# Performance work log

Hardware: AMD Instinct MI355X
Metric: run time of the kernel (lower is better)

Reference implementation:

```python
import jax, jax.numpy as jnp
import numpy as np

EPS = 1e-5

def _binact(x):
    # ReActNet piecewise-polynomial sign with straight-through estimator
    p = jnp.where(x < -1.0, -1.0,
        jnp.where(x < 0.0, x * x + 2.0 * x,
        jnp.where(x < 1.0, -x * x + 2.0 * x, 1.0)))
    return jax.lax.stop_gradient(jnp.sign(x) - p) + p

def _binweight(w):
    # per-output-channel scaling * sign(w), STE through clipped weights
    scale = jax.lax.stop_gradient(jnp.mean(jnp.abs(w), axis=(1, 2, 3), keepdims=True))
    bw = scale * jnp.sign(w)
    cl = jnp.clip(w, -1.0, 1.0)
    return jax.lax.stop_gradient(bw - cl) + cl

def _conv(x, w, stride, pad):
    return jax.lax.conv_general_dilated(x, w, (stride, stride), [(pad, pad), (pad, pad)],
                                        dimension_numbers=('NCHW', 'OIHW', 'NCHW'))

def _bn(x, gamma, beta, mean, var):
    inv = gamma / jnp.sqrt(var + EPS)
    return x * inv[None, :, None, None] + (beta - mean * inv)[None, :, None, None]

def _prelu(x, a):
    return jnp.where(x > 0, x, a[None, :, None, None] * x)

def _bias(x, b):
    return x + b[None, :, None, None]

def setup_inputs() -> dict:
    key = jax.random.key(0)
    ks = jax.random.split(key, 12)
    B, C, H, W = 32, 256, 28, 28
    d = {}
    d['x'] = jax.random.normal(ks[0], (B, C, H, W), jnp.float32)
    d['loss'] = jnp.zeros((), jnp.float32)
    # learnable biases (move11/12/13, move21/22/23)
    for i, name in enumerate(['b11', 'b12', 'b13', 'b21', 'b22', 'b23']):
        d[name] = 0.01 * jax.random.normal(ks[1 + i], (C,), jnp.float32)
    # binary conv weights: 3x3 (C->C, groups=1) and 1x1 (C->C)
    d['w1'] = 0.05 * jax.random.normal(ks[7], (C, C, 3, 3), jnp.float32)
    d['w2'] = 0.05 * jax.random.normal(ks[8], (C, C, 1, 1), jnp.float32)
    # batchnorm params (inference-style running stats)
    d['g1'] = jnp.ones((C,), jnp.float32); d['be1'] = jnp.zeros((C,), jnp.float32)
    d['m1'] = 0.1 * jax.random.normal(ks[9], (C,), jnp.float32)
    d['v1'] = 0.5 + jax.random.uniform(ks[10], (C,), jnp.float32)
    d['g2'] = jnp.ones((C,), jnp.float32); d['be2'] = jnp.zeros((C,), jnp.float32)
    d['m2'] = 0.1 * jax.random.normal(ks[11], (C,), jnp.float32)
    d['v2'] = 0.5 + jax.random.uniform(jax.random.fold_in(key, 99), (C,), jnp.float32)
    # PReLU slopes
    d['a1'] = 0.25 * jnp.ones((C,), jnp.float32)
    d['a2'] = 0.25 * jnp.ones((C,), jnp.float32)
    return d

def reference(x, loss, b11, b12, b13, b21, b22, b23, w1, w2,
              g1, be1, m1, v1, g2, be2, m2, v2, a1, a2):
    # branch 1: bias -> sign act -> 3x3 binary conv -> BN -> residual -> bias/PReLU/bias
    out1 = _binact(_bias(x, b11))
    out1 = _conv(out1, _binweight(w1), 1, 1)
    out1 = _bn(out1, g1, be1, m1, v1)
    out1 = out1 + x  # adaptive_add: shapes match (stride=1, inp==oup)
    out1 = _bias(_prelu(_bias(out1, b12), a1), b13)
    # branch 2: bias -> sign act -> 1x1 binary conv -> BN -> residual -> bias/PReLU/bias
    out2 = _binact(_bias(out1, b21))
    out2 = _conv(out2, _binweight(w2), 1, 0)
    out2 = _bn(out2, g2, be2, m2, v2)
    out2 = out2 + out1
    out2 = _bias(_prelu(_bias(out2, b22), a2), b23)
    return (out2, loss)
```

## Files before the change

### kernel.cpp

```cpp
#include <hip/hip_runtime.h>
#include <hip/hip_bf16.h>


typedef unsigned short u16;
typedef unsigned char  u8;
typedef unsigned int   u32;
typedef unsigned long long u64;
typedef float f32x4 __attribute__((ext_vector_type(4)));
typedef long  long2v __attribute__((ext_vector_type(2)));
typedef int   v8i  __attribute__((ext_vector_type(8)));
typedef float v16f __attribute__((ext_vector_type(16)));

__device__ __forceinline__ float b2f(u16 u) {
  union { unsigned int i; float f; } c; c.i = ((unsigned int)u) << 16; return c.f;
}
__device__ __forceinline__ u16 f2b(float f) {
  unsigned int u = __builtin_bit_cast(unsigned int, f);
  unsigned int r = (u + 0x7FFFu + ((u >> 16) & 1u)) >> 16;
  return (u16)r;
}
__device__ __forceinline__ u32 f2sign4(float v) {
  return (v > 0.f) ? 0x2u : ((v < 0.f) ? 0xAu : 0x0u);
}
__device__ __forceinline__ v8i mkv8(long2v a, long2v b) {
  union { long2v l[2]; v8i v; } u; u.l[0] = a; u.l[1] = b; return u.v;
}

__global__ __launch_bounds__(256) void prep_kernel(
    const float* __restrict__ w1, const float* __restrict__ w2,
    const float* __restrict__ g1, const float* __restrict__ be1,
    const float* __restrict__ m1, const float* __restrict__ v1,
    const float* __restrict__ g2, const float* __restrict__ be2,
    const float* __restrict__ m2, const float* __restrict__ v2,
    u8* __restrict__ w1T, u8* __restrict__ w2T,
    float* __restrict__ ab,
    float* __restrict__ lossdst, const float* __restrict__ lossin)
{
  __shared__ float wrow[2304];
  __shared__ float red[256];
  const int t = threadIdx.x;
  const int blk = blockIdx.x;
  float s = 0.f;
  if (blk < 256) {
    const int o = blk;
    const float4* src = (const float4*)(w1 + o * 2304);
#pragma unroll
    for (int i = 0; i < 3; ++i) {
      int c = i * 256 + t;
      if (c < 576) {
        float4 v = src[c];
        wrow[c * 4 + 0] = v.x; wrow[c * 4 + 1] = v.y;
        wrow[c * 4 + 2] = v.z; wrow[c * 4 + 3] = v.w;
        s += fabsf(v.x) + fabsf(v.y) + fabsf(v.z) + fabsf(v.w);
      }
    }
  } else {
    const int o = blk - 256;
    float v = w2[o * 256 + t];
    wrow[t] = v;
    s = fabsf(v);
  }
  red[t] = s;
  __syncthreads();
  for (int st = 128; st > 0; st >>= 1) { if (t < st) red[t] += red[t + st]; __syncthreads(); }
  if (blk < 256) {
    const int o = blk;
    for (int it = t; it < 288; it += 256) {
      int tap = it >> 5, ci8 = it & 31;
      u32 pack = 0;
#pragma unroll
      for (int k = 0; k < 8; ++k)
        pack |= f2sign4(wrow[(ci8 * 8 + k) * 9 + tap]) << (4 * k);
      int c64 = ci8 >> 3, kh = (ci8 >> 2) & 1, slot = ci8 & 3;
      *(u32*)(w1T + (size_t)((tap * 4 + c64) * 2 + kh) * 4096 + o * 16 + slot * 4) = pack;
    }
    if (t == 0) {
      float scale = red[0] / 2304.f;
      float inv = g1[o] / sqrtf(v1[o] + 1e-5f);
      ab[o]       = scale * inv;
      ab[256 + o] = be1[o] - m1[o] * inv;
    }
  } else {
    const int o = blk - 256;
    if (t < 32) {
      u32 pack = 0;
#pragma unroll
      for (int k = 0; k < 8; ++k)
        pack |= f2sign4(wrow[t * 8 + k]) << (4 * k);
      int c64 = t >> 3, kh = (t >> 2) & 1, slot = t & 3;
      *(u32*)(w2T + (size_t)(c64 * 2 + kh) * 4096 + o * 16 + slot * 4) = pack;
    }
    if (t == 0) {
      float scale = red[0] / 256.f;
      float inv = g2[o] / sqrtf(v2[o] + 1e-5f);
      ab[512 + o] = scale * inv;
      ab[768 + o] = be2[o] - m2[o] * inv;
    }
  }
  if (blk == 0 && t == 0) lossdst[0] = lossin[0];
}

__global__ __launch_bounds__(512, 1) void fused_kernel(
    const float* __restrict__ x, const float* __restrict__ b11,
    const u8* __restrict__ w1T, const u8* __restrict__ w2T,
    const float* __restrict__ ab,
    const float* __restrict__ b12, const float* __restrict__ a1,
    const float* __restrict__ b13, const float* __restrict__ b21,
    const float* __restrict__ b22, const float* __restrict__ a2,
    const float* __restrict__ b23,
    float* __restrict__ dout)
{
  __shared__ __align__(16) u8 win[26112];
  __shared__ float bsh[256];

  const int t = threadIdx.x;
  const int w = t >> 6;
  const int l = t & 63;
  const int l31 = l & 31;
  const int h32 = l >> 5;
  const int mg = w & 1;
  const int ng = w >> 1;
  const int pxblk = blockIdx.x;
  const int img = pxblk / 7;
  const int rowgrp = pxblk % 7;

  float al1[2], bt1[2], pA1[2], pS1[2], pB1[2], p21[2];
  float al2[2], bt2[2], pA2[2], pS2[2], pB2[2];
  int Ov[2];
#pragma unroll
  for (int nf = 0; nf < 2; ++nf) {
    int O = ng * 64 + nf * 32 + l31;
    Ov[nf] = O;
    al1[nf] = ab[O];       bt1[nf] = ab[256 + O];
    al2[nf] = ab[512 + O]; bt2[nf] = ab[768 + O];
    pA1[nf] = b12[O]; pS1[nf] = a1[O]; pB1[nf] = b13[O]; p21[nf] = b21[O];
    pA2[nf] = b22[O]; pS2[nf] = a2[O]; pB2[nf] = b23[O];
  }

  int basepix[2];
#pragma unroll
  for (int mi = 0; mi < 2; ++mi) {
    int pm = (mg * 2 + mi) * 32 + l31;
    int r = (pm * 293) >> 13;
    basepix[mi] = r * 30 + (pm - 28 * r);
  }

  char* wl = (char*)win;

  v16f acc[2][2];
  v16f zero16 = {0.f,0.f,0.f,0.f,0.f,0.f,0.f,0.f,0.f,0.f,0.f,0.f,0.f,0.f,0.f,0.f};
  f32x4 zero4 = {0.f, 0.f, 0.f, 0.f};
  long2v zl2 = {0, 0};
#pragma unroll
  for (int mi = 0; mi < 2; ++mi)
#pragma unroll
    for (int nf = 0; nf < 2; ++nf) acc[mi][nf] = zero16;

  if (t < 256) bsh[t] = b11[t];
#pragma unroll
  for (int i = 0; i < 4; ++i) {
    int c = i * 512 + t;
    if (c < 1632) *(f32x4*)(wl + c * 16) = zero4;
  }
  __syncthreads();

#pragma unroll 1
  for (int wr = 0; wr < 6; ++wr) {
    int r_img = rowgrp * 4 - 1 + wr;
    if ((unsigned)r_img < 28u) {
#pragma unroll
      for (int it = 0; it < 2; ++it) {
        int u = it * 512 + t;
        if (u < 896) {
          int c2 = (u * 9363) >> 16;
          int p4 = u - c2 * 7;
          const float* xb = x + ((size_t)(img * 256 + 2 * c2)) * 784 + r_img * 28 + p4 * 4;
          float4 v0 = *(const float4*)(xb);
          float4 v1 = *(const float4*)(xb + 784);
          float b0v = bsh[2 * c2], b1v = bsh[2 * c2 + 1];
          float lo[4] = {v0.x, v0.y, v0.z, v0.w};
          float hi[4] = {v1.x, v1.y, v1.z, v1.w};
          int pbase = wr * 30 + 1 + p4 * 4;
#pragma unroll
          for (int k = 0; k < 4; ++k) {
            int wp = pbase + k;
            u8 byte = (u8)(f2sign4(lo[k] + b0v) | (f2sign4(hi[k] + b1v) << 4));
            wl[wp * 128 + ((((c2 >> 4) ^ (wp & 7)) << 4) | (c2 & 15))] = byte;
          }
        }
      }
    }
  }
  __syncthreads();

  auto LOADB3 = [&](long2v* dst, int s) {
    int sc = (s < 36) ? s : 0;
    const char* base = (const char*)w1T + (size_t)sc * 8192 + h32 * 4096;
#pragma unroll
    for (int nf = 0; nf < 2; ++nf)
      dst[nf] = *(const long2v*)(base + (ng * 64 + nf * 32 + l31) * 16);
  };
  auto DSA3 = [&](long2v* dst, int s) {
    int sc = (s < 36) ? s : 0;
    int tap = sc >> 2;
    int c64 = sc & 3;
    int ti = (tap * 11) >> 5;
    int tapoff = ti * 30 + (tap - 3 * ti);
    int slot = c64 * 2 + h32;
#pragma unroll
    for (int mi = 0; mi < 2; ++mi) {
      int wp = basepix[mi] + tapoff;
      dst[mi] = *(const long2v*)(wl + wp * 128 + ((slot ^ (wp & 7)) << 4));
    }
  };
  auto COMP = [&](long2v* a, long2v* bv) {
    __builtin_amdgcn_s_setprio(1);
#pragma unroll
    for (int mi = 0; mi < 2; ++mi) {
      v8i a8 = mkv8(a[mi], zl2);
#pragma unroll
      for (int nf = 0; nf < 2; ++nf)
        acc[mi][nf] = __builtin_amdgcn_mfma_scale_f32_32x32x64_f8f6f4(
            a8, mkv8(bv[nf], zl2), acc[mi][nf],
            4, 4,
            0, 0x7F7F7F7Fu, 0, 0x7F7F7F7Fu);
    }
    __builtin_amdgcn_s_setprio(0);
  };

  long2v A0[2], A1[2];
  long2v b0[2], b1[2], b2[2];
  DSA3(A0, 0); LOADB3(b0, 0); LOADB3(b1, 1);
#pragma unroll 1
  for (int i = 0; i < 6; ++i) {
    int p = i * 6;
    LOADB3(b2, p + 2); DSA3(A1, p + 1); COMP(A0, b0);
    LOADB3(b0, p + 3); DSA3(A0, p + 2); COMP(A1, b1);
    LOADB3(b1, p + 4); DSA3(A1, p + 3); COMP(A0, b2);
    LOADB3(b2, p + 5); DSA3(A0, p + 4); COMP(A1, b0);
    LOADB3(b0, p + 6); DSA3(A1, p + 5); COMP(A0, b1);
    LOADB3(b1, p + 7); DSA3(A0, p + 6); COMP(A1, b2);
  }
  __syncthreads();

  u32 pk[2][2][4][2];
#pragma unroll
  for (int mi = 0; mi < 2; ++mi) {
    int m = mg * 2 + mi;
#pragma unroll
    for (int rp = 0; rp < 4; ++rp) {
      int pixbase = m * 32 + 8 * rp + 4 * h32;
      bool valid = (m < 3) || (rp < 2);
#pragma unroll
      for (int nf = 0; nf < 2; ++nf) {
        int O = Ov[nf];
        float xv[4] = {0.f, 0.f, 0.f, 0.f};
        if (valid) {
          int hwm = rowgrp * 112 + pixbase;
          float4 xr = *(const float4*)(x + ((size_t)(img * 256 + O) * 784 + hwm));
          xv[0] = xr.x; xv[1] = xr.y; xv[2] = xr.z; xv[3] = xr.w;
        }
        float o1v[4];
        u32 mynibs = 0;
#pragma unroll
        for (int reg = 0; reg < 4; ++reg) {
          float v = acc[mi][nf][rp * 4 + reg] * al1[nf] + bt1[nf] + xv[reg];
          float t1 = v + pA1[nf];
          t1 = (t1 > 0.f) ? t1 : pS1[nf] * t1;
          o1v[reg] = t1 + pB1[nf];
          mynibs |= f2sign4(o1v[reg] + p21[nf]) << (4 * reg);
        }
        u32 partner = __shfl_xor((int)mynibs, 1);
        if ((l31 & 1) == 0) {
          int c2 = O >> 1;
#pragma unroll
          for (int reg = 0; reg < 4; ++reg) {
            int pix = pixbase + reg;
            u8 byte = (u8)(((mynibs >> (4 * reg)) & 0xF) |
                           (((partner >> (4 * reg)) & 0xF) << 4));
            wl[pix * 128 + ((((c2 >> 4) ^ (pix & 7)) << 4) | (c2 & 15))] = byte;
          }
        }
        pk[mi][nf][rp][0] = (u32)f2b(o1v[0]) | ((u32)f2b(o1v[1]) << 16);
        pk[mi][nf][rp][1] = (u32)f2b(o1v[2]) | ((u32)f2b(o1v[3]) << 16);
      }
    }
  }
#pragma unroll
  for (int mi = 0; mi < 2; ++mi)
#pragma unroll
    for (int nf = 0; nf < 2; ++nf) acc[mi][nf] = zero16;

  asm volatile("s_waitcnt lgkmcnt(0)" ::: "memory");
  __builtin_amdgcn_s_barrier();

  auto LOADB1 = [&](long2v* dst, int sp) {
    const char* base = (const char*)w2T + (size_t)sp * 8192 + h32 * 4096;
#pragma unroll
    for (int nf = 0; nf < 2; ++nf)
      dst[nf] = *(const long2v*)(base + (ng * 64 + nf * 32 + l31) * 16);
  };
  auto DSA1 = [&](long2v* dst, int sp) {
    int slot = sp * 2 + h32;
#pragma unroll
    for (int mi = 0; mi < 2; ++mi) {
      int pm = (mg * 2 + mi) * 32 + l31;
      dst[mi] = *(const long2v*)(wl + pm * 128 + ((slot ^ (pm & 7)) << 4));
    }
  };
  DSA1(A0, 0); LOADB1(b0, 0);
  DSA1(A1, 1); LOADB1(b1, 1); COMP(A0, b0);
  DSA1(A0, 2); LOADB1(b0, 2); COMP(A1, b1);
  DSA1(A1, 3); LOADB1(b1, 3); COMP(A0, b0);
  COMP(A1, b1);

#pragma unroll
  for (int mi = 0; mi < 2; ++mi) {
    int m = mg * 2 + mi;
#pragma unroll
    for (int rp = 0; rp < 4; ++rp) {
      bool valid = (m < 3) || (rp < 2);
      if (!valid) continue;
      int pixbase = m * 32 + 8 * rp + 4 * h32;
      int hwm = rowgrp * 112 + pixbase;
#pragma unroll
      for (int nf = 0; nf < 2; ++nf) {
        int O = Ov[nf];
        float res[4];
        res[0] = b2f((u16)(pk[mi][nf][rp][0] & 0xFFFF));
        res[1] = b2f((u16)(pk[mi][nf][rp][0] >> 16));
        res[2] = b2f((u16)(pk[mi][nf][rp][1] & 0xFFFF));
        res[3] = b2f((u16)(pk[mi][nf][rp][1] >> 16));
        float r4v[4];
#pragma unroll
        for (int reg = 0; reg < 4; ++reg) {
          float v = acc[mi][nf][rp * 4 + reg] * al2[nf] + bt2[nf] + res[reg];
          float t1 = v + pA2[nf];
          t1 = (t1 > 0.f) ? t1 : pS2[nf] * t1;
          r4v[reg] = t1 + pB2[nf];
        }
        float4 r4 = {r4v[0], r4v[1], r4v[2], r4v[3]};
        *(float4*)(dout + ((size_t)(img * 256 + O)) * 784 + hwm) = r4;
      }
    }
  }
}

extern "C" void kernel_launch(void* const* d_in, const int* in_sizes, int n_in,
                              void* d_out, int out_size, void* d_ws, size_t ws_size,
                              hipStream_t stream) {
  const float* x    = (const float*)d_in[0];
  const float* loss = (const float*)d_in[1];
  const float* b11  = (const float*)d_in[2];
  const float* b12  = (const float*)d_in[3];
  const float* b13  = (const float*)d_in[4];
  const float* b21  = (const float*)d_in[5];
  const float* b22  = (const float*)d_in[6];
  const float* b23  = (const float*)d_in[7];
  const float* w1   = (const float*)d_in[8];
  const float* w2   = (const float*)d_in[9];
  const float* g1   = (const float*)d_in[10];
  const float* be1  = (const float*)d_in[11];
  const float* m1   = (const float*)d_in[12];
  const float* v1   = (const float*)d_in[13];
  const float* g2   = (const float*)d_in[14];
  const float* be2  = (const float*)d_in[15];
  const float* m2   = (const float*)d_in[16];
  const float* v2   = (const float*)d_in[17];
  const float* a1   = (const float*)d_in[18];
  const float* a2   = (const float*)d_in[19];

  char* ws = (char*)d_ws;
  u8*    w1T = (u8*)(ws + 0ull);
  u8*    w2T = (u8*)(ws + 294912ull);
  float* ab  = (float*)(ws + 327680ull);

  float* out = (float*)d_out;

  prep_kernel<<<512, 256, 0, stream>>>(w1, w2, g1, be1, m1, v1, g2, be2, m2, v2,
                                       w1T, w2T, ab, out + (out_size - 1), loss);
  fused_kernel<<<224, 512, 0, stream>>>(x, b11, w1T, w2T, ab,
                                        b12, a1, b13, b21, b22, a2, b23, out);
}
```

Baseline: 40.04 us.

## Halve per-block pixel tile to two rows and double the grid

Each block now covers two image rows (56 pixels) instead of four, so the grid doubles from 224 to 448 blocks. Each wave handles one 32-pixel M tile instead of two, which halves the accumulators and LDS use, and launch bounds now allow four blocks per CU. The goal is to fill all CUs of the large GPU (224 blocks underfill it) and raise occupancy so latency hides better. In exchange, each block reloads the full weight stream for fewer pixels, and the one-row halo overhead grows from 6/4 to 4/2 rows.

```diff
diff --git a/kernel.cpp b/kernel.cpp
--- a/kernel.cpp
+++ b/kernel.cpp
@@ -100,7 +100,7 @@
   if (blk == 0 && t == 0) lossdst[0] = lossin[0];
 }
 
-__global__ __launch_bounds__(512, 1) void fused_kernel(
+__global__ __launch_bounds__(512, 4) void fused_kernel(
     const float* __restrict__ x, const float* __restrict__ b11,
     const u8* __restrict__ w1T, const u8* __restrict__ w2T,
     const float* __restrict__ ab,
@@ -110,7 +110,7 @@
     const float* __restrict__ b23,
     float* __restrict__ dout)
 {
-  __shared__ __align__(16) u8 win[26112];
+  __shared__ __align__(16) u8 win[20480];
   __shared__ float bsh[256];
 
   const int t = threadIdx.x;
@@ -118,18 +118,18 @@
   const int l = t & 63;
   const int l31 = l & 31;
   const int h32 = l >> 5;
-  const int mg = w & 1;
-  const int ng = w >> 1;
+  const int m = w & 1;
+  const int npair = w >> 1;
   const int pxblk = blockIdx.x;
-  const int img = pxblk / 7;
-  const int rowgrp = pxblk % 7;
+  const int img = pxblk / 14;
+  const int rowpair = pxblk % 14;
 
   float al1[2], bt1[2], pA1[2], pS1[2], pB1[2], p21[2];
   float al2[2], bt2[2], pA2[2], pS2[2], pB2[2];
   int Ov[2];
 #pragma unroll
   for (int nf = 0; nf < 2; ++nf) {
-    int O = ng * 64 + nf * 32 + l31;
+    int O = npair * 64 + nf * 32 + l31;
     Ov[nf] = O;
     al1[nf] = ab[O];       bt1[nf] = ab[256 + O];
     al2[nf] = ab[512 + O]; bt2[nf] = ab[768 + O];
@@ -137,36 +137,29 @@
     pA2[nf] = b22[O]; pS2[nf] = a2[O]; pB2[nf] = b23[O];
   }
 
-  int basepix[2];
-#pragma unroll
-  for (int mi = 0; mi < 2; ++mi) {
-    int pm = (mg * 2 + mi) * 32 + l31;
-    int r = (pm * 293) >> 13;
-    basepix[mi] = r * 30 + (pm - 28 * r);
-  }
+  const int pm = m * 32 + l31;
+  const int pr = (pm * 293) >> 13;
+  const int basepix = pr * 30 + (pm - 28 * pr);
 
   char* wl = (char*)win;
 
-  v16f acc[2][2];
+  v16f acc[2];
   v16f zero16 = {0.f,0.f,0.f,0.f,0.f,0.f,0.f,0.f,0.f,0.f,0.f,0.f,0.f,0.f,0.f,0.f};
   f32x4 zero4 = {0.f, 0.f, 0.f, 0.f};
   long2v zl2 = {0, 0};
-#pragma unroll
-  for (int mi = 0; mi < 2; ++mi)
-#pragma unroll
-    for (int nf = 0; nf < 2; ++nf) acc[mi][nf] = zero16;
+  acc[0] = zero16; acc[1] = zero16;
 
   if (t < 256) bsh[t] = b11[t];
 #pragma unroll
-  for (int i = 0; i < 4; ++i) {
+  for (int i = 0; i < 3; ++i) {
     int c = i * 512 + t;
-    if (c < 1632) *(f32x4*)(wl + c * 16) = zero4;
+    if (c < 1280) *(f32x4*)(wl + c * 16) = zero4;
   }
   __syncthreads();
 
 #pragma unroll 1
-  for (int wr = 0; wr < 6; ++wr) {
-    int r_img = rowgrp * 4 - 1 + wr;
+  for (int wr = 0; wr < 4; ++wr) {
+    int r_img = rowpair * 2 - 1 + wr;
     if ((unsigned)r_img < 28u) {
 #pragma unroll
       for (int it = 0; it < 2; ++it) {
@@ -198,7 +191,7 @@
     const char* base = (const char*)w1T + (size_t)sc * 8192 + h32 * 4096;
 #pragma unroll
     for (int nf = 0; nf < 2; ++nf)
-      dst[nf] = *(const long2v*)(base + (ng * 64 + nf * 32 + l31) * 16);
+      dst[nf] = *(const long2v*)(base + (npair * 64 + nf * 32 + l31) * 16);
   };
   auto DSA3 = [&](long2v* dst, int s) {
     int sc = (s < 36) ? s : 0;
@@ -207,28 +200,21 @@
     int ti = (tap * 11) >> 5;
     int tapoff = ti * 30 + (tap - 3 * ti);
     int slot = c64 * 2 + h32;
-#pragma unroll
-    for (int mi = 0; mi < 2; ++mi) {
-      int wp = basepix[mi] + tapoff;
-      dst[mi] = *(const long2v*)(wl + wp * 128 + ((slot ^ (wp & 7)) << 4));
-    }
+    int wp = basepix + tapoff;
+    dst[0] = *(const long2v*)(wl + wp * 128 + ((slot ^ (wp & 7)) << 4));
   };
   auto COMP = [&](long2v* a, long2v* bv) {
     __builtin_amdgcn_s_setprio(1);
-#pragma unroll
-    for (int mi = 0; mi < 2; ++mi) {
-      v8i a8 = mkv8(a[mi], zl2);
-#pragma unroll
-      for (int nf = 0; nf < 2; ++nf)
-        acc[mi][nf] = __builtin_amdgcn_mfma_scale_f32_32x32x64_f8f6f4(
-            a8, mkv8(bv[nf], zl2), acc[mi][nf],
-            4, 4,
-            0, 0x7F7F7F7Fu, 0, 0x7F7F7F7Fu);
-    }
+    v8i a8 = mkv8(a[0], zl2);
+#pragma unroll
+    for (int nf = 0; nf < 2; ++nf)
+      acc[nf] = __builtin_amdgcn_mfma_scale_f32_32x32x64_f8f6f4(
+          a8, mkv8(bv[nf], zl2), acc[nf],
+          4, 4, 0, 0x7F7F7F7Fu, 0, 0x7F7F7F7Fu);
     __builtin_amdgcn_s_setprio(0);
   };
 
-  long2v A0[2], A1[2];
+  long2v A0[1], A1[1];
   long2v b0[2], b1[2], b2[2];
   DSA3(A0, 0); LOADB3(b0, 0); LOADB3(b1, 1);
 #pragma unroll 1
@@ -243,53 +229,46 @@
   }
   __syncthreads();
 
-  u32 pk[2][2][4][2];
-#pragma unroll
-  for (int mi = 0; mi < 2; ++mi) {
-    int m = mg * 2 + mi;
-#pragma unroll
-    for (int rp = 0; rp < 4; ++rp) {
-      int pixbase = m * 32 + 8 * rp + 4 * h32;
-      bool valid = (m < 3) || (rp < 2);
-#pragma unroll
-      for (int nf = 0; nf < 2; ++nf) {
-        int O = Ov[nf];
-        float xv[4] = {0.f, 0.f, 0.f, 0.f};
-        if (valid) {
-          int hwm = rowgrp * 112 + pixbase;
-          float4 xr = *(const float4*)(x + ((size_t)(img * 256 + O) * 784 + hwm));
-          xv[0] = xr.x; xv[1] = xr.y; xv[2] = xr.z; xv[3] = xr.w;
+  u32 pk[2][4][2];
+#pragma unroll
+  for (int rp = 0; rp < 4; ++rp) {
+    int pixbase = m * 32 + 8 * rp + 4 * h32;
+    bool valid = (m == 0) || (rp < 3);
+#pragma unroll
+    for (int nf = 0; nf < 2; ++nf) {
+      int O = Ov[nf];
+      float xv[4] = {0.f, 0.f, 0.f, 0.f};
+      if (valid) {
+        int hwm = rowpair * 56 + pixbase;
+        float4 xr = *(const float4*)(x + ((size_t)(img * 256 + O) * 784 + hwm));
+        xv[0] = xr.x; xv[1] = xr.y; xv[2] = xr.z; xv[3] = xr.w;
+      }
+      float o1v[4];
+      u32 mynibs = 0;
+#pragma unroll
+      for (int reg = 0; reg < 4; ++reg) {
+        float v = acc[nf][rp * 4 + reg] * al1[nf] + bt1[nf] + xv[reg];
+        float t1 = v + pA1[nf];
+        t1 = (t1 > 0.f) ? t1 : pS1[nf] * t1;
+        o1v[reg] = t1 + pB1[nf];
+        mynibs |= f2sign4(o1v[reg] + p21[nf]) << (4 * reg);
+      }
+      u32 partner = __shfl_xor((int)mynibs, 1);
+      if ((l31 & 1) == 0) {
+        int c2 = O >> 1;
+#pragma unroll
+        for (int reg = 0; reg < 4; ++reg) {
+          int pix = pixbase + reg;
+          u8 byte = (u8)(((mynibs >> (4 * reg)) & 0xF) |
+                         (((partner >> (4 * reg)) & 0xF) << 4));
+          wl[pix * 128 + ((((c2 >> 4) ^ (pix & 7)) << 4) | (c2 & 15))] = byte;
         }
-        float o1v[4];
-        u32 mynibs = 0;
-#pragma unroll
-        for (int reg = 0; reg < 4; ++reg) {
-          float v = acc[mi][nf][rp * 4 + reg] * al1[nf] + bt1[nf] + xv[reg];
-          float t1 = v + pA1[nf];
-          t1 = (t1 > 0.f) ? t1 : pS1[nf] * t1;
-          o1v[reg] = t1 + pB1[nf];
-          mynibs |= f2sign4(o1v[reg] + p21[nf]) << (4 * reg);
-        }
-        u32 partner = __shfl_xor((int)mynibs, 1);
-        if ((l31 & 1) == 0) {
-          int c2 = O >> 1;
-#pragma unroll
-          for (int reg = 0; reg < 4; ++reg) {
-            int pix = pixbase + reg;
-            u8 byte = (u8)(((mynibs >> (4 * reg)) & 0xF) |
-                           (((partner >> (4 * reg)) & 0xF) << 4));
-            wl[pix * 128 + ((((c2 >> 4) ^ (pix & 7)) << 4) | (c2 & 15))] = byte;
-          }
-        }
-        pk[mi][nf][rp][0] = (u32)f2b(o1v[0]) | ((u32)f2b(o1v[1]) << 16);
-        pk[mi][nf][rp][1] = (u32)f2b(o1v[2]) | ((u32)f2b(o1v[3]) << 16);
-      }
-    }
-  }
-#pragma unroll
-  for (int mi = 0; mi < 2; ++mi)
-#pragma unroll
-    for (int nf = 0; nf < 2; ++nf) acc[mi][nf] = zero16;
+      }
+      pk[nf][rp][0] = (u32)f2b(o1v[0]) | ((u32)f2b(o1v[1]) << 16);
+      pk[nf][rp][1] = (u32)f2b(o1v[2]) | ((u32)f2b(o1v[3]) << 16);
+    }
+  }
+  acc[0] = zero16; acc[1] = zero16;
 
   asm volatile("s_waitcnt lgkmcnt(0)" ::: "memory");
   __builtin_amdgcn_s_barrier();
@@ -298,15 +277,11 @@
     const char* base = (const char*)w2T + (size_t)sp * 8192 + h32 * 4096;
 #pragma unroll
     for (int nf = 0; nf < 2; ++nf)
-      dst[nf] = *(const long2v*)(base + (ng * 64 + nf * 32 + l31) * 16);
+      dst[nf] = *(const long2v*)(base + (npair * 64 + nf * 32 + l31) * 16);
   };
   auto DSA1 = [&](long2v* dst, int sp) {
     int slot = sp * 2 + h32;
-#pragma unroll
-    for (int mi = 0; mi < 2; ++mi) {
-      int pm = (mg * 2 + mi) * 32 + l31;
-      dst[mi] = *(const long2v*)(wl + pm * 128 + ((slot ^ (pm & 7)) << 4));
-    }
+    dst[0] = *(const long2v*)(wl + pm * 128 + ((slot ^ (pm & 7)) << 4));
   };
   DSA1(A0, 0); LOADB1(b0, 0);
   DSA1(A1, 1); LOADB1(b1, 1); COMP(A0, b0);
@@ -315,33 +290,29 @@
   COMP(A1, b1);
 
 #pragma unroll
-  for (int mi = 0; mi < 2; ++mi) {
-    int m = mg * 2 + mi;
-#pragma unroll
-    for (int rp = 0; rp < 4; ++rp) {
-      bool valid = (m < 3) || (rp < 2);
-      if (!valid) continue;
-      int pixbase = m * 32 + 8 * rp + 4 * h32;
-      int hwm = rowgrp * 112 + pixbase;
-#pragma unroll
-      for (int nf = 0; nf < 2; ++nf) {
-        int O = Ov[nf];
-        float res[4];
-        res[0] = b2f((u16)(pk[mi][nf][rp][0] & 0xFFFF));
-        res[1] = b2f((u16)(pk[mi][nf][rp][0] >> 16));
-        res[2] = b2f((u16)(pk[mi][nf][rp][1] & 0xFFFF));
-        res[3] = b2f((u16)(pk[mi][nf][rp][1] >> 16));
-        float r4v[4];
-#pragma unroll
-        for (int reg = 0; reg < 4; ++reg) {
-          float v = acc[mi][nf][rp * 4 + reg] * al2[nf] + bt2[nf] + res[reg];
-          float t1 = v + pA2[nf];
-          t1 = (t1 > 0.f) ? t1 : pS2[nf] * t1;
-          r4v[reg] = t1 + pB2[nf];
-        }
-        float4 r4 = {r4v[0], r4v[1], r4v[2], r4v[3]};
-        *(float4*)(dout + ((size_t)(img * 256 + O)) * 784 + hwm) = r4;
-      }
+  for (int rp = 0; rp < 4; ++rp) {
+    bool valid = (m == 0) || (rp < 3);
+    if (!valid) continue;
+    int pixbase = m * 32 + 8 * rp + 4 * h32;
+    int hwm = rowpair * 56 + pixbase;
+#pragma unroll
+    for (int nf = 0; nf < 2; ++nf) {
+      int O = Ov[nf];
+      float res[4];
+      res[0] = b2f((u16)(pk[nf][rp][0] & 0xFFFF));
+      res[1] = b2f((u16)(pk[nf][rp][0] >> 16));
+      res[2] = b2f((u16)(pk[nf][rp][1] & 0xFFFF));
+      res[3] = b2f((u16)(pk[nf][rp][1] >> 16));
+      float r4v[4];
+#pragma unroll
+      for (int reg = 0; reg < 4; ++reg) {
+        float v = acc[nf][rp * 4 + reg] * al2[nf] + bt2[nf] + res[reg];
+        float t1 = v + pA2[nf];
+        t1 = (t1 > 0.f) ? t1 : pS2[nf] * t1;
+        r4v[reg] = t1 + pB2[nf];
+      }
+      float4 r4 = {r4v[0], r4v[1], r4v[2], r4v[3]};
+      *(float4*)(dout + ((size_t)(img * 256 + O)) * 784 + hwm) = r4;
     }
   }
 }
@@ -379,6 +350,6 @@
 
   prep_kernel<<<512, 256, 0, stream>>>(w1, w2, g1, be1, m1, v1, g2, be2, m2, v2,
                                        w1T, w2T, ab, out + (out_size - 1), loss);
-  fused_kernel<<<224, 512, 0, stream>>>(x, b11, w1T, w2T, ab,
+  fused_kernel<<<448, 512, 0, stream>>>(x, b11, w1T, w2T, ab,
                                         b12, a1, b13, b21, b22, a2, b23, out);
 }
```

After: 41.92 us. 4.7% more time.

## Stage output tile in LDS for coalesced stores and deepen conv pipelines

Applied to the files above, without the earlier changes.

The final output is now written to a large shared-memory tile (116-float stride per channel) and then copied to global memory in contiguous 16-byte chunks per channel row, instead of each lane doing scattered float4 stores. The 3x3 conv main loop switches to a three-deep A-operand register rotation, and the 1x1 conv weights are prefetched into registers before the epilogue of the first conv. This targets uncoalesced global writes and load latency, at the cost of a much larger LDS allocation (about 116 KB), extra barriers, and more registers.

```diff
diff --git a/kernel.cpp b/kernel.cpp
--- a/kernel.cpp
+++ b/kernel.cpp
@@ -110,7 +110,7 @@
     const float* __restrict__ b23,
     float* __restrict__ dout)
 {
-  __shared__ __align__(16) u8 win[26112];
+  __shared__ __align__(16) u8 shmem[118784];
   __shared__ float bsh[256];
 
   const int t = threadIdx.x;
@@ -145,7 +145,7 @@
     basepix[mi] = r * 30 + (pm - 28 * r);
   }
 
-  char* wl = (char*)win;
+  char* wl = (char*)shmem;
 
   v16f acc[2][2];
   v16f zero16 = {0.f,0.f,0.f,0.f,0.f,0.f,0.f,0.f,0.f,0.f,0.f,0.f,0.f,0.f,0.f,0.f};
@@ -228,20 +228,26 @@
     __builtin_amdgcn_s_setprio(0);
   };
 
-  long2v A0[2], A1[2];
+  long2v A0[2], A1[2], A2[2];
   long2v b0[2], b1[2], b2[2];
-  DSA3(A0, 0); LOADB3(b0, 0); LOADB3(b1, 1);
+  DSA3(A0, 0); DSA3(A1, 1); LOADB3(b0, 0); LOADB3(b1, 1);
 #pragma unroll 1
-  for (int i = 0; i < 6; ++i) {
-    int p = i * 6;
-    LOADB3(b2, p + 2); DSA3(A1, p + 1); COMP(A0, b0);
-    LOADB3(b0, p + 3); DSA3(A0, p + 2); COMP(A1, b1);
-    LOADB3(b1, p + 4); DSA3(A1, p + 3); COMP(A0, b2);
-    LOADB3(b2, p + 5); DSA3(A0, p + 4); COMP(A1, b0);
-    LOADB3(b0, p + 6); DSA3(A1, p + 5); COMP(A0, b1);
-    LOADB3(b1, p + 7); DSA3(A0, p + 6); COMP(A1, b2);
-  }
-  __syncthreads();
+  for (int i = 0; i < 12; ++i) {
+    int p = i * 3;
+    LOADB3(b2, p + 2); DSA3(A2, p + 2); COMP(A0, b0);
+    LOADB3(b0, p + 3); DSA3(A0, p + 3); COMP(A1, b1);
+    LOADB3(b1, p + 4); DSA3(A1, p + 4); COMP(A2, b2);
+  }
+  __syncthreads();
+
+  auto LOADB1 = [&](long2v* dst, int sp) {
+    const char* base = (const char*)w2T + (size_t)sp * 8192 + h32 * 4096;
+#pragma unroll
+    for (int nf = 0; nf < 2; ++nf)
+      dst[nf] = *(const long2v*)(base + (ng * 64 + nf * 32 + l31) * 16);
+  };
+  long2v B10[2], B11[2], B12[2], B13[2];
+  LOADB1(B10, 0); LOADB1(B11, 1); LOADB1(B12, 2); LOADB1(B13, 3);
 
   u32 pk[2][2][4][2];
 #pragma unroll
@@ -294,12 +300,6 @@
   asm volatile("s_waitcnt lgkmcnt(0)" ::: "memory");
   __builtin_amdgcn_s_barrier();
 
-  auto LOADB1 = [&](long2v* dst, int sp) {
-    const char* base = (const char*)w2T + (size_t)sp * 8192 + h32 * 4096;
-#pragma unroll
-    for (int nf = 0; nf < 2; ++nf)
-      dst[nf] = *(const long2v*)(base + (ng * 64 + nf * 32 + l31) * 16);
-  };
   auto DSA1 = [&](long2v* dst, int sp) {
     int slot = sp * 2 + h32;
 #pragma unroll
@@ -308,12 +308,15 @@
       dst[mi] = *(const long2v*)(wl + pm * 128 + ((slot ^ (pm & 7)) << 4));
     }
   };
-  DSA1(A0, 0); LOADB1(b0, 0);
-  DSA1(A1, 1); LOADB1(b1, 1); COMP(A0, b0);
-  DSA1(A0, 2); LOADB1(b0, 2); COMP(A1, b1);
-  DSA1(A1, 3); LOADB1(b1, 3); COMP(A0, b0);
-  COMP(A1, b1);
-
+  DSA1(A0, 0);
+  DSA1(A1, 1); COMP(A0, B10);
+  DSA1(A0, 2); COMP(A1, B11);
+  DSA1(A1, 3); COMP(A0, B12);
+  COMP(A1, B13);
+
+  __syncthreads();
+
+  float* outf = (float*)shmem;
 #pragma unroll
   for (int mi = 0; mi < 2; ++mi) {
     int m = mg * 2 + mi;
@@ -322,7 +325,6 @@
       bool valid = (m < 3) || (rp < 2);
       if (!valid) continue;
       int pixbase = m * 32 + 8 * rp + 4 * h32;
-      int hwm = rowgrp * 112 + pixbase;
 #pragma unroll
       for (int nf = 0; nf < 2; ++nf) {
         int O = Ov[nf];
@@ -331,18 +333,29 @@
         res[1] = b2f((u16)(pk[mi][nf][rp][0] >> 16));
         res[2] = b2f((u16)(pk[mi][nf][rp][1] & 0xFFFF));
         res[3] = b2f((u16)(pk[mi][nf][rp][1] >> 16));
-        float r4v[4];
+        f32x4 r4;
 #pragma unroll
         for (int reg = 0; reg < 4; ++reg) {
           float v = acc[mi][nf][rp * 4 + reg] * al2[nf] + bt2[nf] + res[reg];
           float t1 = v + pA2[nf];
           t1 = (t1 > 0.f) ? t1 : pS2[nf] * t1;
-          r4v[reg] = t1 + pB2[nf];
-        }
-        float4 r4 = {r4v[0], r4v[1], r4v[2], r4v[3]};
-        *(float4*)(dout + ((size_t)(img * 256 + O)) * 784 + hwm) = r4;
+          r4[reg] = t1 + pB2[nf];
+        }
+        *(f32x4*)(&outf[O * 116 + pixbase]) = r4;
       }
     }
+  }
+  __syncthreads();
+
+  const size_t obase = (size_t)img * 200704 + (size_t)rowgrp * 112;
+#pragma unroll
+  for (int i = 0; i < 14; ++i) {
+    int u = i * 512 + t;
+    int och = u / 28;
+    int q = u - och * 28;
+    f32x4 v = *(const f32x4*)(&outf[och * 116 + q * 4]);
+    float4 r4 = {v[0], v[1], v[2], v[3]};
+    *(float4*)(dout + obase + (size_t)och * 784 + q * 4) = r4;
   }
 }
 
```

Measured after the change: 39.29 us. Within noise of the previous version (-1.9%).
